# Performance work log

Hardware: AMD Instinct MI355X
Metric: run time of the kernel (lower is better)

Reference implementation:

```python
import jax, jax.numpy as jnp
import numpy as np

EPS = 1e-8  # matches F.cosine_similarity eps clamp

def _cosine_gram(x):
    # row-normalize with eps clamp, then Gram matrix == pairwise cosine similarity
    norms = jnp.maximum(jnp.linalg.norm(x, axis=-1, keepdims=True), EPS)
    xn = x / norms
    return xn @ xn.T  # [N, N]

def setup_inputs() -> dict:
    key = jax.random.key(0)
    k1, k2 = jax.random.split(key)
    N, D = 4096, 512
    return {
        "cosine_distance_latent": jax.random.normal(k1, (N, D), dtype=jnp.float32),
        "mse_latent": jax.random.normal(k2, (N, D), dtype=jnp.float32),
    }

def reference(cosine_distance_latent, mse_latent):
    # cosine distance matrices: (sim - 1) * -1 == 1 - sim
    cd = 1.0 - _cosine_gram(cosine_distance_latent)  # target
    ed = 1.0 - _cosine_gram(mse_latent)              # predicted
    # KL(softmax(cd) || softmax(ed)) per row, then mean
    log_t = jax.nn.log_softmax(cd, axis=-1)
    log_p = jax.nn.log_softmax(ed, axis=-1)
    t = jnp.exp(log_t)
    kl = jnp.sum(t * (log_t - log_p), axis=-1)
    return jnp.mean(kl)
```

## Files before the change

kernel.cpp:

```cpp
#include <hip/hip_runtime.h>
#include <math.h>

#define NROWS 4096
#define DIM   512
#define UNIT_I 128
#define UNIT_J 64
#define NGRAINS 1056
#define KSTEPS (DIM / 32)
#define NSLOT 64

typedef __bf16 bf16x8 __attribute__((ext_vector_type(8)));
typedef float  f32x4  __attribute__((ext_vector_type(4)));

#define GL16(G, L) __builtin_amdgcn_global_load_lds( \
    (const __attribute__((address_space(1))) void*)(G), \
    (__attribute__((address_space(3))) void*)(L), 16, 0, 0)

__global__ __launch_bounds__(256)
void normalize_kernel(const float* __restrict__ X, const float* __restrict__ Y,
                      __bf16* __restrict__ Xn, __bf16* __restrict__ Yn)
{
    const int wid  = threadIdx.x >> 6;
    const int lane = threadIdx.x & 63;
    const int row  = blockIdx.x * 4 + wid;
    const float* src = blockIdx.y ? Y : X;
    __bf16*      dst = blockIdx.y ? Yn : Xn;

    const float4* s4 = reinterpret_cast<const float4*>(src + (size_t)row * DIM);
    float4 v0 = s4[lane * 2 + 0];
    float4 v1 = s4[lane * 2 + 1];
    float ss = v0.x*v0.x + v0.y*v0.y + v0.z*v0.z + v0.w*v0.w
             + v1.x*v1.x + v1.y*v1.y + v1.z*v1.z + v1.w*v1.w;
    #pragma unroll
    for (int m = 1; m < 64; m <<= 1) ss += __shfl_xor(ss, m);
    const float scale = 1.0f / fmaxf(sqrtf(ss), 1e-8f);

    bf16x8 o;
    o[0] = (__bf16)(v0.x * scale); o[1] = (__bf16)(v0.y * scale);
    o[2] = (__bf16)(v0.z * scale); o[3] = (__bf16)(v0.w * scale);
    o[4] = (__bf16)(v1.x * scale); o[5] = (__bf16)(v1.y * scale);
    o[6] = (__bf16)(v1.z * scale); o[7] = (__bf16)(v1.w * scale);
    *reinterpret_cast<bf16x8*>(dst + (size_t)row * DIM + lane * 8) = o;
}

__global__ __launch_bounds__(256, 2)
void gram_kl_kernel(const __bf16* __restrict__ Xn, const __bf16* __restrict__ Yn,
                    float4* __restrict__ partials)
{
    __shared__ char lds[65536];

    const int tid  = threadIdx.x;
    const int wid  = tid >> 6;
    const int lane = tid & 63;
    const int m  = wid >> 1;
    const int iq = wid & 1;

    const int gl = (blockIdx.x & 7) * (NGRAINS / 8) + (blockIdx.x >> 3);
    int p = (int)((sqrtf((float)(4 * gl + 1)) - 1.0f) * 0.5f);
    while ((p + 1) * (p + 2) <= gl) ++p;
    while (p * (p + 1) > gl) --p;
    const int q = gl - p * (p + 1);
    const int i0 = p * UNIT_I;
    const int j0 = q * UNIT_J;
    const int diag = (p == (q >> 1));

    const int xnib = (((lane & 3) ^ ((lane >> 3) & 3)) << 4);
    const int rr = lane >> 2;
    const size_t so_j = ((size_t)(j0 + rr) << 10) + xnib;
    const size_t so_i = ((size_t)(i0 + iq * 64 + rr) << 10) + xnib;

    const char* bx = (const char*)Xn;
    const char* srcM = m ? (const char*)Yn : bx;

    char* const wlds = &lds[wid * 16384];

    auto STAGE = [&](int st, int ks) {
        char* base = wlds + st * 8192;
        const size_t ko = (size_t)ks << 6;
        #pragma unroll
        for (int k2 = 0; k2 < 4; ++k2)
            GL16(srcM + so_j + ((size_t)k2 << 14) + ko, base + k2 * 1024);
        #pragma unroll
        for (int k2 = 0; k2 < 4; ++k2)
            GL16(srcM + so_i + ((size_t)k2 << 14) + ko, base + 4096 + k2 * 1024);
    };

    const int rdx = ((lane & 15) << 6) + ((((lane >> 4) ^ ((lane >> 1) & 3))) << 4);

    f32x4 acc[4][4];
    #pragma unroll
    for (int fj = 0; fj < 4; ++fj)
        #pragma unroll
        for (int fi = 0; fi < 4; ++fi)
            acc[fj][fi] = f32x4{0.f, 0.f, 0.f, 0.f};

    STAGE(0, 0);

    for (int s = 0; s < KSTEPS; ++s) {
        if (s + 1 < KSTEPS) {
            STAGE((s + 1) & 1, s + 1);
            asm volatile("s_waitcnt vmcnt(8)" ::: "memory");
        } else {
            asm volatile("s_waitcnt vmcnt(0)" ::: "memory");
        }

        const char* base = wlds + (s & 1) * 8192;
        bf16x8 aJ[4], bI[4];
        #pragma unroll
        for (int fj = 0; fj < 4; ++fj)
            aJ[fj] = *reinterpret_cast<const bf16x8*>(base + fj * 1024 + rdx);
        #pragma unroll
        for (int fi = 0; fi < 4; ++fi)
            bI[fi] = *reinterpret_cast<const bf16x8*>(base + 4096 + fi * 1024 + rdx);

        __builtin_amdgcn_s_setprio(1);
        #pragma unroll
        for (int fj = 0; fj < 4; ++fj)
            #pragma unroll
            for (int fi = 0; fi < 4; ++fi)
                acc[fj][fi] = __builtin_amdgcn_mfma_f32_16x16x32_bf16(aJ[fj], bI[fi], acc[fj][fi], 0, 0, 0);
        __builtin_amdgcn_s_setprio(0);
    }

    char*  chunk = &lds[0];
    float* jpart = reinterpret_cast<float*>(&lds[8192]);

    const int sub = lane >> 4;
    float Si[4] = {0,0,0,0}, Ui[4] = {0,0,0,0}, Vi[4] = {0,0,0,0}, Qi[4] = {0,0,0,0};

    __syncthreads();

    #pragma unroll
    for (int fj = 0; fj < 4; ++fj) {
        if (m == 1) {
            #pragma unroll
            for (int fi = 0; fi < 4; ++fi)
                *reinterpret_cast<f32x4*>(chunk + iq * 4096 + fi * 1024 + lane * 16) = acc[fj][fi];
        }
        __syncthreads();
        if (m == 0) {
            float js[4][4];
            #pragma unroll
            for (int r = 0; r < 4; ++r) { js[r][0]=0; js[r][1]=0; js[r][2]=0; js[r][3]=0; }
            #pragma unroll
            for (int fi = 0; fi < 4; ++fi) {
                const f32x4 pb = *reinterpret_cast<const f32x4*>(chunk + iq * 4096 + fi * 1024 + lane * 16);
                #pragma unroll
                for (int r = 0; r < 4; ++r) {
                    const float a = -acc[fj][fi][r];
                    const float b = -pb[r];
                    const float ea = __expf(a);
                    const float eb = __expf(b);
                    Si[fi] += ea; Ui[fi] += ea * a; Vi[fi] += ea * b; Qi[fi] += eb;
                    js[r][0] += ea; js[r][1] += ea * a; js[r][2] += ea * b; js[r][3] += eb;
                }
            }
            if (!diag) {
                #pragma unroll
                for (int r = 0; r < 4; ++r)
                    #pragma unroll
                    for (int c = 0; c < 4; ++c) {
                        #pragma unroll
                        for (int mk = 1; mk <= 8; mk <<= 1)
                            js[r][c] += __shfl_xor(js[r][c], mk);
                    }
                if ((lane & 15) == 0) {
                    #pragma unroll
                    for (int r = 0; r < 4; ++r) {
                        const int j = fj * 16 + sub * 4 + r;
                        #pragma unroll
                        for (int c = 0; c < 4; ++c)
                            jpart[(iq * 64 + j) * 4 + c] = js[r][c];
                    }
                }
            }
        }
        __syncthreads();
    }

    if (m == 0) {
        #pragma unroll
        for (int fi = 0; fi < 4; ++fi) {
            #pragma unroll
            for (int mk = 16; mk <= 32; mk <<= 1) {
                Si[fi] += __shfl_xor(Si[fi], mk);
                Ui[fi] += __shfl_xor(Ui[fi], mk);
                Vi[fi] += __shfl_xor(Vi[fi], mk);
                Qi[fi] += __shfl_xor(Qi[fi], mk);
            }
        }
        if (lane < 16) {
            #pragma unroll
            for (int fi = 0; fi < 4; ++fi) {
                const int row = i0 + iq * 64 + fi * 16 + lane;
                partials[(size_t)row * NSLOT + q] = float4{Si[fi], Ui[fi], Vi[fi], Qi[fi]};
            }
        }
    }
    __syncthreads();

    if (!diag && wid == 0) {
        const int j = lane;
        const int mslot = (q >> 1) + p + 1;
        float4 v;
        v.x = jpart[(0 * 64 + j) * 4 + 0] + jpart[(1 * 64 + j) * 4 + 0];
        v.y = jpart[(0 * 64 + j) * 4 + 1] + jpart[(1 * 64 + j) * 4 + 1];
        v.z = jpart[(0 * 64 + j) * 4 + 2] + jpart[(1 * 64 + j) * 4 + 2];
        v.w = jpart[(0 * 64 + j) * 4 + 3] + jpart[(1 * 64 + j) * 4 + 3];
        partials[(size_t)(j0 + j) * NSLOT + mslot] = v;
    }
}

__global__ __launch_bounds__(256)
void merge_kernel(const float4* __restrict__ partials, float* __restrict__ blocksum)
{
    __shared__ float w[4];
    const int row = blockIdx.x * 256 + threadIdx.x;
    const int nsl = (row >> 7) + 33;
    float S = 0.f, U = 0.f, V = 0.f, Q = 0.f;
    for (int s = 0; s < nsl; ++s) {
        const float4 pp = partials[(size_t)row * NSLOT + s];
        S += pp.x; U += pp.y; V += pp.z; Q += pp.w;
    }
    float kl = (U - V) / S - logf(S) + logf(Q);
    #pragma unroll
    for (int mm = 1; mm < 64; mm <<= 1) kl += __shfl_xor(kl, mm);
    if ((threadIdx.x & 63) == 0) w[threadIdx.x >> 6] = kl;
    __syncthreads();
    if (threadIdx.x == 0) blocksum[blockIdx.x] = w[0] + w[1] + w[2] + w[3];
}

__global__ __launch_bounds__(64)
void reduce_kernel(const float* __restrict__ blocksum, float* __restrict__ out)
{
    float v = (threadIdx.x < 16) ? blocksum[threadIdx.x] : 0.f;
    #pragma unroll
    for (int mm = 1; mm < 16; mm <<= 1) v += __shfl_xor(v, mm);
    if (threadIdx.x == 0) out[0] = v / (float)NROWS;
}

extern "C" void kernel_launch(void* const* d_in, const int* in_sizes, int n_in,
                              void* d_out, int out_size, void* d_ws, size_t ws_size,
                              hipStream_t stream)
{
    const float* X = (const float*)d_in[0];
    const float* Y = (const float*)d_in[1];
    float* out = (float*)d_out;

    char* ws = (char*)d_ws;
    const size_t mat_bytes = (size_t)NROWS * DIM * sizeof(__bf16);
    __bf16* Xn = (__bf16*)ws;
    __bf16* Yn = (__bf16*)(ws + mat_bytes);
    float4* partials = (float4*)(ws + 2 * mat_bytes);
    float* blocksum = (float*)(ws + 2 * mat_bytes + (size_t)NROWS * NSLOT * sizeof(float4));

    normalize_kernel<<<dim3(NROWS / 4, 2), 256, 0, stream>>>(X, Y, Xn, Yn);
    gram_kl_kernel<<<NGRAINS, 256, 0, stream>>>(Xn, Yn, partials);
    merge_kernel<<<NROWS / 256, 256, 0, stream>>>(partials, blocksum);
    reduce_kernel<<<1, 64, 0, stream>>>(blocksum, out);
}
```

Baseline: 72.27 us.

## Load MFMA operands directly from global into registers, dropping LDS staging

Replaces the per-wave global_load_lds double-buffered staging and the LDS fragment reads with direct global-to-register bf16x8 loads, double-buffered in registers, and fully unrolls the k loop. LDS shrinks to the 10 KB needed for the epilogue, and launch bounds rise to 3 blocks per CU to raise occupancy. The trade-off is that fragments are read from global/L2 in a less coalesced pattern (16-byte pieces across 16 rows), and the register double buffering adds pressure under the tighter launch bound.

```diff
diff --git a/kernel.cpp b/kernel.cpp
--- a/kernel.cpp
+++ b/kernel.cpp
@@ -12,10 +12,6 @@
 typedef __bf16 bf16x8 __attribute__((ext_vector_type(8)));
 typedef float  f32x4  __attribute__((ext_vector_type(4)));
 
-#define GL16(G, L) __builtin_amdgcn_global_load_lds( \
-    (const __attribute__((address_space(1))) void*)(G), \
-    (__attribute__((address_space(3))) void*)(L), 16, 0, 0)
-
 __global__ __launch_bounds__(256)
 void normalize_kernel(const float* __restrict__ X, const float* __restrict__ Y,
                       __bf16* __restrict__ Xn, __bf16* __restrict__ Yn)
@@ -43,11 +39,11 @@
     *reinterpret_cast<bf16x8*>(dst + (size_t)row * DIM + lane * 8) = o;
 }
 
-__global__ __launch_bounds__(256, 2)
+__global__ __launch_bounds__(256, 3)
 void gram_kl_kernel(const __bf16* __restrict__ Xn, const __bf16* __restrict__ Yn,
                     float4* __restrict__ partials)
 {
-    __shared__ char lds[65536];
+    __shared__ char lds[10240];
 
     const int tid  = threadIdx.x;
     const int wid  = tid >> 6;
@@ -64,28 +60,10 @@
     const int j0 = q * UNIT_J;
     const int diag = (p == (q >> 1));
 
-    const int xnib = (((lane & 3) ^ ((lane >> 3) & 3)) << 4);
-    const int rr = lane >> 2;
-    const size_t so_j = ((size_t)(j0 + rr) << 10) + xnib;
-    const size_t so_i = ((size_t)(i0 + iq * 64 + rr) << 10) + xnib;
-
-    const char* bx = (const char*)Xn;
-    const char* srcM = m ? (const char*)Yn : bx;
-
-    char* const wlds = &lds[wid * 16384];
-
-    auto STAGE = [&](int st, int ks) {
-        char* base = wlds + st * 8192;
-        const size_t ko = (size_t)ks << 6;
-        #pragma unroll
-        for (int k2 = 0; k2 < 4; ++k2)
-            GL16(srcM + so_j + ((size_t)k2 << 14) + ko, base + k2 * 1024);
-        #pragma unroll
-        for (int k2 = 0; k2 < 4; ++k2)
-            GL16(srcM + so_i + ((size_t)k2 << 14) + ko, base + 4096 + k2 * 1024);
-    };
-
-    const int rdx = ((lane & 15) << 6) + ((((lane >> 4) ^ ((lane >> 1) & 3))) << 4);
+    const char* srcM = m ? (const char*)Yn : (const char*)Xn;
+
+    const size_t jb = ((size_t)(j0 + (lane & 15)) << 10) + (size_t)((lane >> 4) << 4);
+    const size_t ib = ((size_t)(i0 + iq * 64 + (lane & 15)) << 10) + (size_t)((lane >> 4) << 4);
 
     f32x4 acc[4][4];
     #pragma unroll
@@ -94,31 +72,27 @@
         for (int fi = 0; fi < 4; ++fi)
             acc[fj][fi] = f32x4{0.f, 0.f, 0.f, 0.f};
 
-    STAGE(0, 0);
-
+    bf16x8 fJ[2][4], fI[2][4];
+
+    auto LOAD = [&](int buf, int s) {
+        #pragma unroll
+        for (int f = 0; f < 4; ++f) {
+            fJ[buf][f] = *reinterpret_cast<const bf16x8*>(srcM + jb + ((size_t)f << 14) + ((size_t)s << 6));
+            fI[buf][f] = *reinterpret_cast<const bf16x8*>(srcM + ib + ((size_t)f << 14) + ((size_t)s << 6));
+        }
+    };
+
+    LOAD(0, 0);
+    #pragma unroll
     for (int s = 0; s < KSTEPS; ++s) {
-        if (s + 1 < KSTEPS) {
-            STAGE((s + 1) & 1, s + 1);
-            asm volatile("s_waitcnt vmcnt(8)" ::: "memory");
-        } else {
-            asm volatile("s_waitcnt vmcnt(0)" ::: "memory");
-        }
-
-        const char* base = wlds + (s & 1) * 8192;
-        bf16x8 aJ[4], bI[4];
+        if (s + 1 < KSTEPS) LOAD((s + 1) & 1, s + 1);
+
+        __builtin_amdgcn_s_setprio(1);
         #pragma unroll
         for (int fj = 0; fj < 4; ++fj)
-            aJ[fj] = *reinterpret_cast<const bf16x8*>(base + fj * 1024 + rdx);
-        #pragma unroll
-        for (int fi = 0; fi < 4; ++fi)
-            bI[fi] = *reinterpret_cast<const bf16x8*>(base + 4096 + fi * 1024 + rdx);
-
-        __builtin_amdgcn_s_setprio(1);
-        #pragma unroll
-        for (int fj = 0; fj < 4; ++fj)
             #pragma unroll
             for (int fi = 0; fi < 4; ++fi)
-                acc[fj][fi] = __builtin_amdgcn_mfma_f32_16x16x32_bf16(aJ[fj], bI[fi], acc[fj][fi], 0, 0, 0);
+                acc[fj][fi] = __builtin_amdgcn_mfma_f32_16x16x32_bf16(fJ[s & 1][fj], fI[s & 1][fi], acc[fj][fi], 0, 0, 0);
         __builtin_amdgcn_s_setprio(0);
     }
 
```

Measured after the change: 101.7 us. 1.41x slower.
